# Performance work log

Hardware: AMD Instinct MI355X
Metric: run time of the kernel (lower is better)

The kernel has to match this reference:

```python
import jax, jax.numpy as jnp
import numpy as np

B, S, D, H = 2, 2048, 512, 8
DK = D // H
MASK_VALUE = -1e9


def setup_inputs() -> dict:
    key = jax.random.key(0)
    ks = jax.random.split(key, 12)
    scale = 1.0 / np.sqrt(D)
    inp = {
        "query": jax.random.normal(ks[0], (B, S, D), jnp.float32),
        "key": jax.random.normal(ks[1], (B, S, D), jnp.float32),
        "value": jax.random.normal(ks[2], (B, S, D), jnp.float32),
        # causal mask, broadcastable over batch and heads
        "mask": jnp.tril(jnp.ones((S, S), jnp.int32))[None, None, :, :],
        "Wq": jax.random.normal(ks[3], (D, D), jnp.float32) * scale,
        "bq": jax.random.normal(ks[4], (D,), jnp.float32) * scale,
        "Wk": jax.random.normal(ks[5], (D, D), jnp.float32) * scale,
        "bk": jax.random.normal(ks[6], (D,), jnp.float32) * scale,
        "Wv": jax.random.normal(ks[7], (D, D), jnp.float32) * scale,
        "bv": jax.random.normal(ks[8], (D,), jnp.float32) * scale,
        "Wo": jax.random.normal(ks[9], (D, D), jnp.float32) * scale,
        "bo": jax.random.normal(ks[10], (D,), jnp.float32) * scale,
    }
    return inp


def reference(query, key, value, mask, Wq, bq, Wk, bk, Wv, bv, Wo, bo):
    # linear projections (torch Linear: x @ W.T + b)
    q = query @ Wq.T + bq
    k = key @ Wk.T + bk
    v = value @ Wv.T + bv
    # split heads: [B,S,D] -> [B,H,S,DK]
    q = q.reshape(B, S, H, DK).transpose(0, 2, 1, 3)
    k = k.reshape(B, S, H, DK).transpose(0, 2, 1, 3)
    v = v.reshape(B, S, H, DK).transpose(0, 2, 1, 3)
    # scaled dot-product attention with explicit [B,H,S,S] score matrix
    scores = jnp.einsum("bhqd,bhkd->bhqk", q, k) / jnp.sqrt(jnp.float32(DK))
    scores = jnp.where(mask == 0, jnp.float32(MASK_VALUE), scores)
    attn = jax.nn.softmax(scores, axis=-1)
    x = jnp.einsum("bhqk,bhkd->bhqd", attn, v)
    # merge heads: [B,H,S,DK] -> [B,S,D]
    x = x.transpose(0, 2, 1, 3).reshape(B, S, D)
    return x @ Wo.T + bo
```

## Files before the change

kernel.cpp:

```cpp
#include <hip/hip_runtime.h>
#include <hip/hip_bf16.h>

#define B_   2
#define S_   2048
#define D_   512
#define H_   8
#define DK_  64
#define M_   (B_*S_)

typedef float  floatx4 __attribute__((ext_vector_type(4)));
typedef __bf16 bf16x8  __attribute__((ext_vector_type(8)));

#define MFMA16x16x32(a,b,c) __builtin_amdgcn_mfma_f32_16x16x32_bf16((a),(b),(c),0,0,0)

static __device__ __forceinline__ void load_lds16(const void* g, void* l) {
  __builtin_amdgcn_global_load_lds(
      (const __attribute__((address_space(1))) void*)g,
      (__attribute__((address_space(3))) void*)l,
      16, 0, 0);
}

__global__ __launch_bounds__(256) void cvt_inputs(
    const float* __restrict__ w0, const float* __restrict__ w1,
    const float* __restrict__ w2, const float* __restrict__ w3,
    const float* __restrict__ x0, const float* __restrict__ x1,
    const float* __restrict__ x2,
    __bf16* __restrict__ out)
{
  const int idx = (blockIdx.x * 256 + threadIdx.x) * 4;
  const float* src;
  int off;
  if (idx < 1048576) {
    src = (idx < 524288) ? ((idx < 262144) ? w0 : w1)
                         : ((idx < 786432) ? w2 : w3);
    off = idx & 0x3FFFF;
  } else {
    const int i2 = idx - 1048576;
    const int xs = i2 >> 21;
    src = (xs == 0) ? x0 : (xs == 1) ? x1 : x2;
    off = i2 & 0x1FFFFF;
  }
  float4 v = *(const float4*)(src + off);
  __bf16* o = out + idx;
  o[0]=(__bf16)v.x; o[1]=(__bf16)v.y; o[2]=(__bf16)v.z; o[3]=(__bf16)v.w;
}


__global__ __launch_bounds__(256) void proj_qkv(
    const __bf16* __restrict__ Xb, const __bf16* __restrict__ Wball,
    const float* __restrict__ bq, const float* __restrict__ bk, const float* __restrict__ bv,
    __bf16* __restrict__ Qb, __bf16* __restrict__ Kb, __bf16* __restrict__ Vtb)
{
  __shared__ __align__(16) __bf16 smem[12288];

  const int z = blockIdx.z;
  const __bf16* X    = Xb + (size_t)z * (M_*D_);
  const __bf16* W    = Wball + (size_t)z * (D_*D_);
  const float*  bias = (z==0) ? bq : (z==1) ? bk : bv;

  const int m0 = blockIdx.x * 64;
  const int n0 = blockIdx.y * 128;
  const int tid  = threadIdx.x;
  const int w    = tid >> 6;
  const int lane = tid & 63;
  const int lcol = lane & 15;
  const int quad = lane >> 4;
  const int wm = w & 1, wn = w >> 1;

  floatx4 zero = {0.f,0.f,0.f,0.f};
  floatx4 acc[2][4];
#pragma unroll
  for (int i = 0; i < 2; ++i)
#pragma unroll
    for (int nt = 0; nt < 4; ++nt) acc[i][nt] = zero;

  auto stage = [&](int bsel, int k0) {
    {
      const int u = w*64 + lane;
      load_lds16(X + (size_t)(m0 + (u >> 2))*D_ + k0 + (u & 3)*8,
                 (char*)(smem + bsel*2048) + w*1024);
    }
#pragma unroll
    for (int j = 0; j < 2; ++j) {
      const int u = (j*4 + w)*64 + lane;
      load_lds16(W + (size_t)(n0 + (u >> 2))*D_ + k0 + (u & 3)*8,
                 (char*)(smem + 4096 + bsel*4096) + (j*4 + w)*1024);
    }
  };

  stage(0, 0);
  for (int it = 0; it < 16; ++it) {
    __syncthreads();
    if (it + 1 < 16) stage((it+1)&1, (it+1)*32);
    const __bf16* ab = smem + (it&1)*2048;
    const __bf16* bb = smem + 4096 + (it&1)*4096;
    bf16x8 af[2], bf[4];
#pragma unroll
    for (int i = 0; i < 2; ++i)
      af[i] = *(const bf16x8*)(ab + (wm*32 + i*16 + lcol)*32 + quad*8);
#pragma unroll
    for (int nt = 0; nt < 4; ++nt)
      bf[nt] = *(const bf16x8*)(bb + (wn*64 + nt*16 + lcol)*32 + quad*8);
#pragma unroll
    for (int i = 0; i < 2; ++i)
#pragma unroll
      for (int nt = 0; nt < 4; ++nt)
        acc[i][nt] = MFMA16x16x32(af[i], bf[nt], acc[i][nt]);
  }

  __syncthreads();
#pragma unroll
  for (int nt = 0; nt < 4; ++nt) {
    const int n = n0 + wn*64 + nt*16 + lcol;
    const float bias_n = bias[n];
    const int h_l = (n >> 6) & 1;
    const int dk  = n & 63;
#pragma unroll
    for (int i = 0; i < 2; ++i)
#pragma unroll
      for (int r = 0; r < 4; ++r) {
        const int m = m0 + wm*32 + i*16 + quad*4 + r;
        const float val = acc[i][nt][r] + bias_n;
        const int klo = m & 63;
        int off;
        if (z == 0) {
          off = klo*64 + dk;
        } else if (z == 1) {
          off = (((klo>>4)*2 + (dk>>5))*64 + ((dk>>3)&3)*16 + (klo&15))*8 + (dk&7);
        } else {
          off = (((dk>>4)*2 + (klo>>5))*64 + ((klo>>3)&3)*16 + (dk&15))*8 + (klo&7);
        }
        smem[h_l*4096 + off] = (__bf16)val;
      }
  }
  __syncthreads();

  __bf16* dst = (z==0) ? Qb : (z==1) ? Kb : Vtb;
  const int bb2 = m0 >> 11;
  const int hh0 = n0 >> 6;
  const int cc0 = (m0 & 2047) >> 6;
#pragma unroll
  for (int it2 = 0; it2 < 4; ++it2) {
    const int u = it2*256 + tid;
    const int p = u >> 9, o = u & 511;
    const size_t base = ((size_t)(bb2*H_ + hh0 + p))*(S_*DK_) + (size_t)cc0*4096;
    *(bf16x8*)(dst + base + o*8) = *(const bf16x8*)(smem + p*4096 + o*8);
  }
}

__global__ __launch_bounds__(256) void attn_fwd(
    const __bf16* __restrict__ Qb, const __bf16* __restrict__ Kb,
    const __bf16* __restrict__ Vtb, __bf16* __restrict__ attnb,
    __bf16* __restrict__ Pb, float* __restrict__ Lb)
{
  __shared__ __align__(16) __bf16 kbuf[2][4096];
  __shared__ __align__(16) __bf16 vbuf[2][4096];
  __shared__ __align__(16) __bf16 pbuf[4][16*72];

  const int tid  = threadIdx.x;
  const int w    = tid >> 6;
  const int lane = tid & 63;
  const int lcol = lane & 15;
  const int quad = lane >> 4;
  const int hh = blockIdx.y;
  const int bb = blockIdx.z;

  const int wid = blockIdx.x;
  int t, s;
  if (wid < 8)       { t = wid;                  s = 0; }
  else if (wid < 24) { int u = wid - 8;  t = 8  + (u>>1); s = u & 1; }
  else if (wid < 48) { int u = wid - 24; int q3 = u/3; t = 16 + q3; s = u - 3*q3; }
  else               { int u = wid - 48; t = 24 + (u>>2); s = u & 3; }
  const bool single = (wid < 8);

  const int cbeg = s*8;
  const int cend = (cbeg + 8 < t + 1) ? (cbeg + 8) : (t + 1);
  const int q0  = t * 64;
  const int qr0 = q0 + w*16;

  const __bf16* Qp = Qb  + (size_t)(bb*H_ + hh) * S_ * DK_;
  const __bf16* Kp = Kb  + (size_t)(bb*H_ + hh) * S_ * DK_;
  const __bf16* Vp = Vtb + (size_t)(bb*H_ + hh) * DK_ * S_;

  const bf16x8 aq0 = *(const bf16x8*)(Qp + (size_t)(qr0 + lcol)*DK_ + quad*8);
  const bf16x8 aq1 = *(const bf16x8*)(Qp + (size_t)(qr0 + lcol)*DK_ + 32 + quad*8);

  floatx4 zero = {0.f,0.f,0.f,0.f};
  floatx4 acc[4] = {zero, zero, zero, zero};
  float lsum[4] = {0.f, 0.f, 0.f, 0.f};

  auto stage_chunk = [&](int bsel, int c) {
    const char* ksrc = (const char*)(Kp + (size_t)c * 4096);
    const char* vsrc = (const char*)(Vp + (size_t)c * 4096);
#pragma unroll
    for (int j = 0; j < 2; ++j) {
      const int off = w*2048 + j*1024;
      load_lds16(ksrc + off + lane*16, (char*)kbuf[bsel] + off);
      load_lds16(vsrc + off + lane*16, (char*)vbuf[bsel] + off);
    }
  };

  stage_chunk(0, cbeg);
  for (int c = cbeg; c < cend; ++c) {
    __syncthreads();
    if (c + 1 < cend) stage_chunk((c - cbeg + 1)&1, c+1);
    const int bsel = (c - cbeg) & 1;
    const int k0 = c * 64;
    const __bf16* kb = kbuf[bsel];
    const __bf16* vb = vbuf[bsel];

    floatx4 sc[4];
#pragma unroll
    for (int nt = 0; nt < 4; ++nt) {
      bf16x8 kf0 = *(const bf16x8*)(kb + (nt*2+0)*512 + lane*8);
      bf16x8 kf1 = *(const bf16x8*)(kb + (nt*2+1)*512 + lane*8);
      sc[nt] = MFMA16x16x32(aq1, kf1, MFMA16x16x32(aq0, kf0, zero));
    }

    const bool edge = (k0 + 63 > qr0);
#pragma unroll
    for (int nt = 0; nt < 4; ++nt) {
#pragma unroll
      for (int r = 0; r < 4; ++r) {
        float p = exp2f(sc[nt][r] * 0.18033688011112042f);
        if (edge) {
          const int qrow = qr0 + quad*4 + r;
          if (k0 + nt*16 + lcol > qrow) p = 0.f;
        }
        lsum[r] += p;
        pbuf[w][(quad*4 + r)*72 + nt*16 + lcol] = (__bf16)p;
      }
    }
    asm volatile("s_waitcnt lgkmcnt(0)" ::: "memory");

    const bf16x8 pa0 = *(const bf16x8*)(&pbuf[w][lcol*72 + quad*8]);
    const bf16x8 pa1 = *(const bf16x8*)(&pbuf[w][lcol*72 + 32 + quad*8]);
#pragma unroll
    for (int nt = 0; nt < 4; ++nt) {
      bf16x8 vf0 = *(const bf16x8*)(vb + (nt*2+0)*512 + lane*8);
      bf16x8 vf1 = *(const bf16x8*)(vb + (nt*2+1)*512 + lane*8);
      acc[nt] = MFMA16x16x32(pa0, vf0, acc[nt]);
      acc[nt] = MFMA16x16x32(pa1, vf1, acc[nt]);
    }
  }

  float tv[4];
#pragma unroll
  for (int r = 0; r < 4; ++r) {
    float v = lsum[r];
    v += __shfl_xor(v, 1, 16);
    v += __shfl_xor(v, 2, 16);
    v += __shfl_xor(v, 4, 16);
    v += __shfl_xor(v, 8, 16);
    tv[r] = v;
  }

  if (single) {
#pragma unroll
    for (int nt = 0; nt < 4; ++nt)
#pragma unroll
      for (int r = 0; r < 4; ++r) {
        const int q = qr0 + quad*4 + r;
        attnb[((size_t)(bb*S_ + q)) * D_ + hh*DK_ + nt*16 + lcol] =
            (__bf16)(acc[nt][r] / tv[r]);
      }
  } else {
    const int g = t >> 3;
    const int basec = (g == 2) ? 16 : ((g == 3) ? 40 : 0);
    const int pidx = (bb*H_ + hh)*72 + basec + (t - 8*g)*(g + 1) + s;

#pragma unroll
    for (int nt = 0; nt < 4; ++nt)
#pragma unroll
      for (int r = 0; r < 4; ++r)
        pbuf[w][(quad*4 + r)*72 + nt*16 + lcol] = (__bf16)acc[nt][r];
    asm volatile("s_waitcnt lgkmcnt(0)" ::: "memory");

    __bf16* pdst = Pb + (size_t)pidx*4096 + w*16*64;
#pragma unroll
    for (int i = 0; i < 2; ++i) {
      const int unit = i*64 + lane;
      const int row = unit >> 3, grp = unit & 7;
      *(bf16x8*)(pdst + row*64 + grp*8) =
          *(const bf16x8*)(&pbuf[w][row*72 + grp*8]);
    }
    if (lcol == 0) {
#pragma unroll
      for (int r = 0; r < 4; ++r)
        Lb[(size_t)pidx*64 + w*16 + quad*4 + r] = tv[r];
    }
  }
}

__global__ __launch_bounds__(256) void attn_reduce(
    const __bf16* __restrict__ Pb, const float* __restrict__ Lb,
    __bf16* __restrict__ attnb)
{
  const int t  = 8 + blockIdx.x;
  const int bh = blockIdx.y;
  const int bb = bh >> 3, hh = bh & 7;
  const int g = t >> 3;
  const int basec = (g == 2) ? 16 : ((g == 3) ? 40 : 0);
  const int nseg = g + 1;
  const int pidx0 = bh*72 + basec + (t - 8*g)*nseg;

#pragma unroll
  for (int i = 0; i < 2; ++i) {
    const int unit = i*256 + threadIdx.x;
    const int row = unit >> 3, grp = unit & 7;
    float sum[8] = {0,0,0,0,0,0,0,0};
    float l = 0.f;
    for (int s2 = 0; s2 < nseg; ++s2) {
      bf16x8 v = *(const bf16x8*)(Pb + (size_t)(pidx0 + s2)*4096 + row*64 + grp*8);
#pragma unroll
      for (int j = 0; j < 8; ++j) sum[j] += (float)v[j];
      l += Lb[(size_t)(pidx0 + s2)*64 + row];
    }
    const float rinv = 1.0f / l;
    bf16x8 o;
#pragma unroll
    for (int j = 0; j < 8; ++j) o[j] = (__bf16)(sum[j] * rinv);
    *(bf16x8*)(attnb + ((size_t)(bb*S_ + t*64 + row))*D_ + hh*DK_ + grp*8) = o;
  }
}

__global__ __launch_bounds__(256) void proj_out(
    const __bf16* __restrict__ attnb, const __bf16* __restrict__ Wob,
    const float* __restrict__ bo, float* __restrict__ out)
{
  __shared__ __align__(16) __bf16 smem[12288];

  const int m0 = blockIdx.x * 64;
  const int n0 = blockIdx.y * 128;
  const int tid  = threadIdx.x;
  const int w    = tid >> 6;
  const int lane = tid & 63;
  const int lcol = lane & 15;
  const int quad = lane >> 4;
  const int wm = w & 1, wn = w >> 1;

  floatx4 zero = {0.f,0.f,0.f,0.f};
  floatx4 acc[2][4];
#pragma unroll
  for (int i = 0; i < 2; ++i)
#pragma unroll
    for (int nt = 0; nt < 4; ++nt) acc[i][nt] = zero;

  auto stage = [&](int bsel, int k0) {
    {
      const int u = w*64 + lane;
      load_lds16(attnb + (size_t)(m0 + (u >> 2))*D_ + k0 + (u & 3)*8,
                 (char*)(smem + bsel*2048) + w*1024);
    }
#pragma unroll
    for (int j = 0; j < 2; ++j) {
      const int u = (j*4 + w)*64 + lane;
      load_lds16(Wob + (size_t)(n0 + (u >> 2))*D_ + k0 + (u & 3)*8,
                 (char*)(smem + 4096 + bsel*4096) + (j*4 + w)*1024);
    }
  };

  stage(0, 0);
  for (int it = 0; it < 16; ++it) {
    __syncthreads();
    if (it + 1 < 16) stage((it+1)&1, (it+1)*32);
    const __bf16* ab = smem + (it&1)*2048;
    const __bf16* bb = smem + 4096 + (it&1)*4096;
    bf16x8 af[2], bf[4];
#pragma unroll
    for (int i = 0; i < 2; ++i)
      af[i] = *(const bf16x8*)(ab + (wm*32 + i*16 + lcol)*32 + quad*8);
#pragma unroll
    for (int nt = 0; nt < 4; ++nt)
      bf[nt] = *(const bf16x8*)(bb + (wn*64 + nt*16 + lcol)*32 + quad*8);
#pragma unroll
    for (int i = 0; i < 2; ++i)
#pragma unroll
      for (int nt = 0; nt < 4; ++nt)
        acc[i][nt] = MFMA16x16x32(af[i], bf[nt], acc[i][nt]);
  }

#pragma unroll
  for (int nt = 0; nt < 4; ++nt) {
    const int n = n0 + wn*64 + nt*16 + lcol;
    const float bias_n = bo[n];
#pragma unroll
    for (int i = 0; i < 2; ++i)
#pragma unroll
      for (int r = 0; r < 4; ++r) {
        const int m = m0 + wm*32 + i*16 + quad*4 + r;
        out[(size_t)m * D_ + n] = acc[i][nt][r] + bias_n;
      }
  }
}

extern "C" void kernel_launch(void* const* d_in, const int* in_sizes, int n_in,
                              void* d_out, int out_size, void* d_ws, size_t ws_size,
                              hipStream_t stream) {
  const float* q_in = (const float*)d_in[0];
  const float* k_in = (const float*)d_in[1];
  const float* v_in = (const float*)d_in[2];
  const float* Wq = (const float*)d_in[4];
  const float* bq = (const float*)d_in[5];
  const float* Wk = (const float*)d_in[6];
  const float* bk = (const float*)d_in[7];
  const float* Wv = (const float*)d_in[8];
  const float* bv = (const float*)d_in[9];
  const float* Wo = (const float*)d_in[10];
  const float* bo = (const float*)d_in[11];
  float* out = (float*)d_out;

  __bf16* ws    = (__bf16*)d_ws;
  __bf16* Qb    = ws;
  __bf16* Kb    = ws + 1*2097152;
  __bf16* Vtb   = ws + 2*2097152;
  __bf16* attnb = ws + 3*2097152;
  __bf16* Wb    = ws + 4*2097152;
  __bf16* Xb    = Wb + 4*262144;

  __bf16* Pb = Xb;
  float*  Lb = (float*)(Xb + 1152*4096);

  cvt_inputs<<<dim3(7168), dim3(256), 0, stream>>>(
      Wq, Wk, Wv, Wo, q_in, k_in, v_in, Wb);

  proj_qkv<<<dim3(M_/64, D_/128, 3), dim3(256), 0, stream>>>(
      Xb, Wb, bq, bk, bv, Qb, Kb, Vtb);

  attn_fwd<<<dim3(80, H_, B_), dim3(256), 0, stream>>>(
      Qb, Kb, Vtb, attnb, Pb, Lb);

  attn_reduce<<<dim3(24, 16), dim3(256), 0, stream>>>(Pb, Lb, attnb);

  proj_out<<<dim3(M_/64, D_/128), dim3(256), 0, stream>>>(
      attnb, Wb + 3*262144, bo, out);
}
```

Baseline: 164.1 us.

## Fuse input conversion into QKV GEMM and split-KV reduce into output projection

```diff
diff --git a/kernel.cpp b/kernel.cpp
--- a/kernel.cpp
+++ b/kernel.cpp
@@ -20,26 +20,28 @@
       16, 0, 0);
 }
 
-__global__ __launch_bounds__(256) void cvt_inputs(
+static __device__ __forceinline__ bf16x8 cvt8(float4 a, float4 b) {
+  bf16x8 r;
+  r[0]=(__bf16)a.x; r[1]=(__bf16)a.y; r[2]=(__bf16)a.z; r[3]=(__bf16)a.w;
+  r[4]=(__bf16)b.x; r[5]=(__bf16)b.y; r[6]=(__bf16)b.z; r[7]=(__bf16)b.w;
+  return r;
+}
+
+static __device__ __forceinline__ int part_idx(int bh, int t, int s) {
+  const int g = t >> 3;
+  const int basec = (g == 2) ? 16 : ((g == 3) ? 40 : 0);
+  return bh*72 + basec + (t - 8*g)*(g + 1) + s;
+}
+
+__global__ __launch_bounds__(256) void cvt_weights(
     const float* __restrict__ w0, const float* __restrict__ w1,
     const float* __restrict__ w2, const float* __restrict__ w3,
-    const float* __restrict__ x0, const float* __restrict__ x1,
-    const float* __restrict__ x2,
     __bf16* __restrict__ out)
 {
   const int idx = (blockIdx.x * 256 + threadIdx.x) * 4;
-  const float* src;
-  int off;
-  if (idx < 1048576) {
-    src = (idx < 524288) ? ((idx < 262144) ? w0 : w1)
-                         : ((idx < 786432) ? w2 : w3);
-    off = idx & 0x3FFFF;
-  } else {
-    const int i2 = idx - 1048576;
-    const int xs = i2 >> 21;
-    src = (xs == 0) ? x0 : (xs == 1) ? x1 : x2;
-    off = i2 & 0x1FFFFF;
-  }
+  const float* src = (idx < 524288) ? ((idx < 262144) ? w0 : w1)
+                                    : ((idx < 786432) ? w2 : w3);
+  const int off = idx & 0x3FFFF;
   float4 v = *(const float4*)(src + off);
   __bf16* o = out + idx;
   o[0]=(__bf16)v.x; o[1]=(__bf16)v.y; o[2]=(__bf16)v.z; o[3]=(__bf16)v.w;
@@ -47,14 +49,15 @@
 
 
 __global__ __launch_bounds__(256) void proj_qkv(
-    const __bf16* __restrict__ Xb, const __bf16* __restrict__ Wball,
+    const float* __restrict__ q_in, const float* __restrict__ k_in,
+    const float* __restrict__ v_in, const __bf16* __restrict__ Wball,
     const float* __restrict__ bq, const float* __restrict__ bk, const float* __restrict__ bv,
     __bf16* __restrict__ Qb, __bf16* __restrict__ Kb, __bf16* __restrict__ Vtb)
 {
   __shared__ __align__(16) __bf16 smem[12288];
 
   const int z = blockIdx.z;
-  const __bf16* X    = Xb + (size_t)z * (M_*D_);
+  const float*  X32  = (z==0) ? q_in : (z==1) ? k_in : v_in;
   const __bf16* W    = Wball + (size_t)z * (D_*D_);
   const float*  bias = (z==0) ? bq : (z==1) ? bk : bv;
 
@@ -67,6 +70,10 @@
   const int quad = lane >> 4;
   const int wm = w & 1, wn = w >> 1;
 
+  const int au  = tid;
+  const int arow = au >> 2, ac8 = (au & 3) * 8;
+  const float* xsrc = X32 + (size_t)(m0 + arow)*D_ + ac8;
+
   floatx4 zero = {0.f,0.f,0.f,0.f};
   floatx4 acc[2][4];
 #pragma unroll
@@ -74,12 +81,7 @@
 #pragma unroll
     for (int nt = 0; nt < 4; ++nt) acc[i][nt] = zero;
 
-  auto stage = [&](int bsel, int k0) {
-    {
-      const int u = w*64 + lane;
-      load_lds16(X + (size_t)(m0 + (u >> 2))*D_ + k0 + (u & 3)*8,
-                 (char*)(smem + bsel*2048) + w*1024);
-    }
+  auto stageB = [&](int bsel, int k0) {
 #pragma unroll
     for (int j = 0; j < 2; ++j) {
       const int u = (j*4 + w)*64 + lane;
@@ -88,10 +90,21 @@
     }
   };
 
-  stage(0, 0);
+  float4 f0, f1;
+  stageB(0, 0);
+  f0 = *(const float4*)(xsrc);
+  f1 = *(const float4*)(xsrc + 4);
+  *(bf16x8*)(smem + au*8) = cvt8(f0, f1);
+
   for (int it = 0; it < 16; ++it) {
     __syncthreads();
-    if (it + 1 < 16) stage((it+1)&1, (it+1)*32);
+    const bool havenext = (it + 1 < 16);
+    float4 g0, g1;
+    if (havenext) {
+      stageB((it+1)&1, (it+1)*32);
+      g0 = *(const float4*)(xsrc + (it+1)*32);
+      g1 = *(const float4*)(xsrc + (it+1)*32 + 4);
+    }
     const __bf16* ab = smem + (it&1)*2048;
     const __bf16* bb = smem + 4096 + (it&1)*4096;
     bf16x8 af[2], bf[4];
@@ -106,6 +119,8 @@
 #pragma unroll
       for (int nt = 0; nt < 4; ++nt)
         acc[i][nt] = MFMA16x16x32(af[i], bf[nt], acc[i][nt]);
+    if (havenext)
+      *(bf16x8*)(smem + ((it+1)&1)*2048 + au*8) = cvt8(g0, g1);
   }
 
   __syncthreads();
@@ -265,9 +280,7 @@
             (__bf16)(acc[nt][r] / tv[r]);
       }
   } else {
-    const int g = t >> 3;
-    const int basec = (g == 2) ? 16 : ((g == 3) ? 40 : 0);
-    const int pidx = (bb*H_ + hh)*72 + basec + (t - 8*g)*(g + 1) + s;
+    const int pidx = part_idx(bb*H_ + hh, t, s);
 
 #pragma unroll
     for (int nt = 0; nt < 4; ++nt)
@@ -292,40 +305,9 @@
   }
 }
 
-__global__ __launch_bounds__(256) void attn_reduce(
-    const __bf16* __restrict__ Pb, const float* __restrict__ Lb,
-    __bf16* __restrict__ attnb)
-{
-  const int t  = 8 + blockIdx.x;
-  const int bh = blockIdx.y;
-  const int bb = bh >> 3, hh = bh & 7;
-  const int g = t >> 3;
-  const int basec = (g == 2) ? 16 : ((g == 3) ? 40 : 0);
-  const int nseg = g + 1;
-  const int pidx0 = bh*72 + basec + (t - 8*g)*nseg;
-
-#pragma unroll
-  for (int i = 0; i < 2; ++i) {
-    const int unit = i*256 + threadIdx.x;
-    const int row = unit >> 3, grp = unit & 7;
-    float sum[8] = {0,0,0,0,0,0,0,0};
-    float l = 0.f;
-    for (int s2 = 0; s2 < nseg; ++s2) {
-      bf16x8 v = *(const bf16x8*)(Pb + (size_t)(pidx0 + s2)*4096 + row*64 + grp*8);
-#pragma unroll
-      for (int j = 0; j < 8; ++j) sum[j] += (float)v[j];
-      l += Lb[(size_t)(pidx0 + s2)*64 + row];
-    }
-    const float rinv = 1.0f / l;
-    bf16x8 o;
-#pragma unroll
-    for (int j = 0; j < 8; ++j) o[j] = (__bf16)(sum[j] * rinv);
-    *(bf16x8*)(attnb + ((size_t)(bb*S_ + t*64 + row))*D_ + hh*DK_ + grp*8) = o;
-  }
-}
-
 __global__ __launch_bounds__(256) void proj_out(
-    const __bf16* __restrict__ attnb, const __bf16* __restrict__ Wob,
+    const __bf16* __restrict__ attnb, const __bf16* __restrict__ Pb,
+    const float* __restrict__ Lb, const __bf16* __restrict__ Wob,
     const float* __restrict__ bo, float* __restrict__ out)
 {
   __shared__ __align__(16) __bf16 smem[12288];
@@ -339,6 +321,16 @@
   const int quad = lane >> 4;
   const int wm = w & 1, wn = w >> 1;
 
+  const int bb  = m0 >> 11;
+  const int t   = (m0 & 2047) >> 6;
+  const bool direct = (t < 8);
+  const int g = t >> 3;
+  const int nseg = g + 1;
+
+  const int au  = tid;
+  const int arow = au >> 2;
+  const int ac8l = (au & 3) * 8;
+
   floatx4 zero = {0.f,0.f,0.f,0.f};
   floatx4 acc[2][4];
 #pragma unroll
@@ -346,12 +338,7 @@
 #pragma unroll
     for (int nt = 0; nt < 4; ++nt) acc[i][nt] = zero;
 
-  auto stage = [&](int bsel, int k0) {
-    {
-      const int u = w*64 + lane;
-      load_lds16(attnb + (size_t)(m0 + (u >> 2))*D_ + k0 + (u & 3)*8,
-                 (char*)(smem + bsel*2048) + w*1024);
-    }
+  auto stageB = [&](int bsel, int k0) {
 #pragma unroll
     for (int j = 0; j < 2; ++j) {
       const int u = (j*4 + w)*64 + lane;
@@ -359,25 +346,75 @@
                  (char*)(smem + 4096 + bsel*4096) + (j*4 + w)*1024);
     }
   };
-
-  stage(0, 0);
+  auto stageA_direct = [&](int bsel, int k0) {
+    load_lds16(attnb + (size_t)(m0 + arow)*D_ + k0 + ac8l,
+               (char*)(smem + bsel*2048) + w*1024);
+  };
+
+  bf16x8 pv[4];
+  float  pl[4];
+  auto loadA_part = [&](int k0) {
+    const int hh = k0 >> 6;
+    const int cblk = k0 & 63;
+    const int pidx0 = part_idx(bb*H_ + hh, t, 0);
+#pragma unroll 4
+    for (int s2 = 0; s2 < 4; ++s2) {
+      if (s2 < nseg) {
+        pv[s2] = *(const bf16x8*)(Pb + (size_t)(pidx0 + s2)*4096
+                                   + arow*64 + cblk + ac8l);
+        pl[s2] = Lb[(size_t)(pidx0 + s2)*64 + arow];
+      }
+    }
+  };
+  auto storeA_part = [&](int bsel) {
+    float sum[8] = {0,0,0,0,0,0,0,0};
+    float l = 0.f;
+#pragma unroll 4
+    for (int s2 = 0; s2 < 4; ++s2) {
+      if (s2 < nseg) {
+#pragma unroll
+        for (int j = 0; j < 8; ++j) sum[j] += (float)pv[s2][j];
+        l += pl[s2];
+      }
+    }
+    const float rinv = 1.0f / l;
+    bf16x8 o;
+#pragma unroll
+    for (int j = 0; j < 8; ++j) o[j] = (__bf16)(sum[j] * rinv);
+    *(bf16x8*)(smem + bsel*2048 + au*8) = o;
+  };
+
+  stageB(0, 0);
+  if (direct) {
+    stageA_direct(0, 0);
+  } else {
+    loadA_part(0);
+    storeA_part(0);
+  }
+
   for (int it = 0; it < 16; ++it) {
     __syncthreads();
-    if (it + 1 < 16) stage((it+1)&1, (it+1)*32);
+    const bool havenext = (it + 1 < 16);
+    if (havenext) {
+      stageB((it+1)&1, (it+1)*32);
+      if (direct) stageA_direct((it+1)&1, (it+1)*32);
+      else        loadA_part((it+1)*32);
+    }
     const __bf16* ab = smem + (it&1)*2048;
-    const __bf16* bb = smem + 4096 + (it&1)*4096;
+    const __bf16* bbp = smem + 4096 + (it&1)*4096;
     bf16x8 af[2], bf[4];
 #pragma unroll
     for (int i = 0; i < 2; ++i)
       af[i] = *(const bf16x8*)(ab + (wm*32 + i*16 + lcol)*32 + quad*8);
 #pragma unroll
     for (int nt = 0; nt < 4; ++nt)
-      bf[nt] = *(const bf16x8*)(bb + (wn*64 + nt*16 + lcol)*32 + quad*8);
+      bf[nt] = *(const bf16x8*)(bbp + (wn*64 + nt*16 + lcol)*32 + quad*8);
 #pragma unroll
     for (int i = 0; i < 2; ++i)
 #pragma unroll
       for (int nt = 0; nt < 4; ++nt)
         acc[i][nt] = MFMA16x16x32(af[i], bf[nt], acc[i][nt]);
+    if (havenext && !direct) storeA_part((it+1)&1);
   }
 
 #pragma unroll
@@ -416,22 +453,17 @@
   __bf16* Vtb   = ws + 2*2097152;
   __bf16* attnb = ws + 3*2097152;
   __bf16* Wb    = ws + 4*2097152;
-  __bf16* Xb    = Wb + 4*262144;
-
-  __bf16* Pb = Xb;
-  float*  Lb = (float*)(Xb + 1152*4096);
-
-  cvt_inputs<<<dim3(7168), dim3(256), 0, stream>>>(
-      Wq, Wk, Wv, Wo, q_in, k_in, v_in, Wb);
+  __bf16* Pb    = Wb + 4*262144;
+  float*  Lb    = (float*)(Pb + 1152*4096);
+
+  cvt_weights<<<dim3(1024), dim3(256), 0, stream>>>(Wq, Wk, Wv, Wo, Wb);
 
   proj_qkv<<<dim3(M_/64, D_/128, 3), dim3(256), 0, stream>>>(
-      Xb, Wb, bq, bk, bv, Qb, Kb, Vtb);
+      q_in, k_in, v_in, Wb, bq, bk, bv, Qb, Kb, Vtb);
 
   attn_fwd<<<dim3(80, H_, B_), dim3(256), 0, stream>>>(
       Qb, Kb, Vtb, attnb, Pb, Lb);
 
-  attn_reduce<<<dim3(24, 16), dim3(256), 0, stream>>>(Pb, Lb, attnb);
-
   proj_out<<<dim3(M_/64, D_/128), dim3(256), 0, stream>>>(
-      attnb, Wb + 3*262144, bo, out);
-}
+      attnb, Pb, Lb, Wb + 3*262144, bo, out);
+}
```

After: 166.5 us. No clear change (+1.5%).
